# Optimization experiments

Measured on AMD Instinct MI355X. Metric: run time of the kernel, lower is better.

## Reference

```python
import jax, jax.numpy as jnp
import numpy as np

IMG_SIZE = 500
FM = 31
RATIOS = [1.0, 2.0, 0.5]
SCALES = [128, 256, 512]
PRE_NMS_TOPN = 6000
POST_NMS_TOPN = 1500
IOU_THRESHOLD = 0.7
VARIANCES = (0.1, 0.1, 0.2, 0.2)
BATCH = 64
TOTAL_ANCHORS = FM * FM * len(RATIOS) * len(SCALES)  # 8649


def generate_anchors():
    # normalized [y1, x1, y2, x2] anchors on a FM x FM grid
    stride = 1.0 / FM
    ctr = (np.arange(FM, dtype=np.float32) + 0.5) * stride
    cx, cy = np.meshgrid(ctr, ctr)
    centers = np.stack([cy.ravel(), cx.ravel()], axis=-1)  # [FM*FM, 2] (cy, cx)
    hs, ws = [], []
    for scale in SCALES:
        for ratio in RATIOS:
            ws.append((scale * np.sqrt(ratio)) / IMG_SIZE)
            hs.append((scale / np.sqrt(ratio)) / IMG_SIZE)
    hw = np.stack([np.array(hs, np.float32), np.array(ws, np.float32)], axis=-1)  # [9, 2]
    mins = centers[:, None, :] - hw[None] / 2.0
    maxs = centers[:, None, :] + hw[None] / 2.0
    boxes = np.concatenate([mins, maxs], axis=-1).reshape(-1, 4)  # [A, 4]
    return np.clip(boxes, 0.0, 1.0).astype(np.float32)


def delta_to_bbox(anchors, deltas):
    # anchors: [A,4], deltas: [B,A,4] (dy, dx, dh, dw) -> [B,A,4] (y1,x1,y2,x2)
    anc_h = anchors[:, 2] - anchors[:, 0]
    anc_w = anchors[:, 3] - anchors[:, 1]
    anc_cy = anchors[:, 0] + 0.5 * anc_h
    anc_cx = anchors[:, 1] + 0.5 * anc_w
    h = jnp.exp(deltas[..., 2]) * anc_h
    w = jnp.exp(deltas[..., 3]) * anc_w
    cy = deltas[..., 0] * anc_h + anc_cy
    cx = deltas[..., 1] * anc_w + anc_cx
    return jnp.stack([cy - 0.5 * h, cx - 0.5 * w, cy + 0.5 * h, cx + 0.5 * w], axis=-1)


def pairwise_iou_one_vs_all(sel_box, boxes):
    # sel_box: [B,1,4], boxes: [B,N,4] -> iou [B,N]
    y1 = jnp.maximum(sel_box[..., 0], boxes[..., 0])
    x1 = jnp.maximum(sel_box[..., 1], boxes[..., 1])
    y2 = jnp.minimum(sel_box[..., 2], boxes[..., 2])
    x2 = jnp.minimum(sel_box[..., 3], boxes[..., 3])
    inter = jnp.maximum(y2 - y1, 0.0) * jnp.maximum(x2 - x1, 0.0)
    area_s = (sel_box[..., 2] - sel_box[..., 0]) * (sel_box[..., 3] - sel_box[..., 1])
    area_b = (boxes[..., 2] - boxes[..., 0]) * (boxes[..., 3] - boxes[..., 1])
    return inter / (area_s + area_b - inter + 1e-9)


def batched_greedy_nms(boxes, scores, max_out, iou_threshold):
    # boxes [B,N,4], scores [B,N]; greedy NMS, vectorized over batch, scan over picks
    B, N, _ = boxes.shape

    def step(active, _):
        masked = jnp.where(active, scores, -jnp.inf)            # [B,N]
        idx = jnp.argmax(masked, axis=1)                         # [B]
        sel_score = jnp.take_along_axis(masked, idx[:, None], axis=1)[:, 0]
        sel_box = jnp.take_along_axis(boxes, idx[:, None, None], axis=1)  # [B,1,4]
        iou = pairwise_iou_one_vs_all(sel_box, boxes)            # [B,N]
        active = active & (iou <= iou_threshold)
        valid = jnp.isfinite(sel_score)
        out_box = jnp.where(valid[:, None], sel_box[:, 0, :], 0.0)
        out_score = jnp.where(valid, sel_score, 0.0)
        return active, (out_box, out_score)

    active0 = jnp.ones((B, N), dtype=bool)
    _, (out_boxes, out_scores) = jax.lax.scan(step, active0, None, length=max_out)
    out_boxes = jnp.transpose(out_boxes, (1, 0, 2))   # [B,max_out,4]
    out_scores = jnp.transpose(out_scores, (1, 0))    # [B,max_out]
    # tf.image.combined_non_max_suppression clips output boxes to [0,1] by default
    return jnp.clip(out_boxes, 0.0, 1.0), out_scores


def setup_inputs() -> dict:
    key = jax.random.key(0)
    k1, k2, k3 = jax.random.split(key, 3)
    rpn_bbox_deltas = jax.random.normal(k1, (BATCH, FM, FM, 36), dtype=jnp.float32)
    rpn_probs = jax.random.uniform(k2, (BATCH, FM, FM, 9), dtype=jnp.float32)
    gt_labels = jax.random.randint(k3, (BATCH, 10), 0, 20).astype(jnp.int64)
    anchors = jnp.asarray(generate_anchors())
    return {"rpn_bbox_deltas": rpn_bbox_deltas, "rpn_probs": rpn_probs,
            "gt_labels": gt_labels, "anchors": anchors}


def reference(rpn_bbox_deltas, rpn_probs, gt_labels, anchors):
    B = rpn_bbox_deltas.shape[0]
    A = anchors.shape[0]
    variances = jnp.asarray(VARIANCES, dtype=rpn_bbox_deltas.dtype)
    deltas = rpn_bbox_deltas.reshape(B, A, 4) * variances
    probs = rpn_probs.reshape(B, A)
    rpn_bboxes = delta_to_bbox(anchors, deltas)              # [B,A,4]
    top_scores, top_idx = jax.lax.top_k(probs, PRE_NMS_TOPN)  # sorted desc
    top_boxes = jnp.take_along_axis(rpn_bboxes, top_idx[:, :, None], axis=1)
    roi_bboxes, roi_scores = batched_greedy_nms(top_boxes, top_scores,
                                                POST_NMS_TOPN, IOU_THRESHOLD)
    return roi_bboxes, roi_scores
```

## Files before the change

kernel.cpp:

```cpp
#include <hip/hip_runtime.h>
#include <math.h>

typedef unsigned int u32;
typedef unsigned short u16;
typedef unsigned long long u64;

#define BATCH 64
#define A_TOT 8649
#define TOPN  6000
#define POST  1500
#define NB    4096
#define NT    512
#define NWAVE 8
#define NSLOT 12
#define NCHUNK 94
#define HOR   16u
#define ENTSTEP 64u
#define DONEBIT 0x80000000u
#define CNTMASK 0x7FFFFFFFu
#define GUARD_MAX (1 << 18)

#define LDS_BYTES 106496

__global__ __launch_bounds__(NT, 2) void roibbox_kernel(
    const float* __restrict__ deltas,
    const float* __restrict__ probs,
    const float* __restrict__ anchors,
    float* __restrict__ out)
{
    #pragma clang fp contract(off)
    __shared__ alignas(16) char smem[LDS_BYTES];
    u64*    keysL   = (u64*)   (smem + 0);
    u32*    bucketA = (u32*)   (smem + 69632);
    u32*    bucketB = (u32*)   (smem + 86016);
    u32*    stemp   = (u32*)   (smem + 102400);
    float4* ringL   = (float4*)(smem + 69632);
    u16*    ppL     = (u16*)   (smem + 93632);
    u32*    ctrlP   = (u32*)   (smem + 105632);
    u32*    ctrlF   = (u32*)   (smem + 105636);
    u32*    bmL     = (u32*)   (smem + 105640);

    const int tid = threadIdx.x;
    const int b   = blockIdx.x;
    const u32 lane = (u32)tid & 63u;
    const u32 w    = (u32)tid >> 6;
    const float* pb = probs + (size_t)b * A_TOT;

    #pragma unroll
    for (int i = 0; i < NB/NT; ++i) bucketA[tid + i*NT] = 0u;
    __syncthreads();

    for (int j = tid; j < A_TOT; j += NT) {
        float s = pb[j];
        int bkt = (int)(s * (float)NB);
        bkt = (NB-1) - min(max(bkt, 0), NB-1);
        atomicAdd(&bucketA[bkt], 1u);
    }
    __syncthreads();

    {
        int base8 = tid << 3;
        u32 c[8]; u32 ms = 0;
        #pragma unroll
        for (int i = 0; i < 8; ++i) { c[i] = bucketA[base8+i]; ms += c[i]; }
        stemp[tid] = ms;
        __syncthreads();
        int src = 0;
        for (int off = 1; off < NT; off <<= 1) {
            u32 v = stemp[src*NT + tid];
            if (tid >= off) v += stemp[src*NT + tid - off];
            stemp[(src^1)*NT + tid] = v;
            __syncthreads();
            src ^= 1;
        }
        u32 excl = stemp[src*NT + tid] - ms;
        #pragma unroll
        for (int i = 0; i < 8; ++i) {
            bucketA[base8+i] = excl; bucketB[base8+i] = excl; excl += c[i];
        }
    }
    __syncthreads();

    for (int j = tid; j < A_TOT; j += NT) {
        float s = pb[j];
        int bkt = (int)(s * (float)NB);
        bkt = (NB-1) - min(max(bkt, 0), NB-1);
        u32 pos = atomicAdd(&bucketB[bkt], 1u);
        keysL[pos] = ((u64)__float_as_uint(s) << 32) | (u64)(~(u32)j);
    }
    __syncthreads();

    for (int bkt = tid; bkt < NB; bkt += NT) {
        int begin = (int)bucketA[bkt], end = (int)bucketB[bkt];
        for (int k = begin + 1; k < end; ++k) {
            u64 key = keysL[k];
            int m = k - 1;
            while (m >= begin && keysL[m] < key) { keysL[m+1] = keysL[m]; --m; }
            keysL[m+1] = key;
        }
    }
    __syncthreads();

    float ry1[NSLOT], rx1[NSLOT], ry2[NSLOT], rx2[NSLOT], rA[NSLOT];
    u32 mask = 0;
    #pragma unroll
    for (int i = 0; i < NSLOT; ++i) {
        u32 s = (u32)i*8u + w;
        u32 r = s*64u + lane;
        ry1[i]=0.f; rx1[i]=0.f; ry2[i]=0.f; rx2[i]=0.f; rA[i]=0.f;
        if (s < NCHUNK && r < TOPN) {
            u64 k = keysL[r];
            u32 aidx = ~((u32)k);
            float4 av = *(const float4*)(anchors + (size_t)aidx * 4);
            float4 dv = *(const float4*)(deltas + ((size_t)b * A_TOT + aidx) * 4);
            float d0 = dv.x*0.1f, d1 = dv.y*0.1f, d2 = dv.z*0.2f, d3 = dv.w*0.2f;
            float ah = av.z - av.x, aw = av.w - av.y;
            float acy = av.x + 0.5f*ah, acx = av.y + 0.5f*aw;
            float h  = (float)exp((double)d2) * ah;
            float wd = (float)exp((double)d3) * aw;
            float cy = d0*ah + acy;
            float cx = d1*aw + acx;
            ry1[i] = cy - 0.5f*h;  rx1[i] = cx - 0.5f*wd;
            ry2[i] = cy + 0.5f*h;  rx2[i] = cx + 0.5f*wd;
            rA[i]  = (ry2[i]-ry1[i])*(rx2[i]-rx1[i]);
            mask |= 1u << i;
        }
    }

    for (int j = tid; j < TOPN/2; j += NT) ((u32*)ppL)[j] = 0xFFFFFFFFu;
    if (tid == 0) { *ctrlP = 0u; *ctrlF = 0u; bmL[0] = 0u; bmL[1] = 0u; bmL[2] = 0xC0000000u; }
    __syncthreads();

    const double MTHR = (double)0.7f + 0x1p-25;

    auto scanNext = [&](u32 from) -> u32 {
        for (u32 k = from >> 5; k < 3u; ++k) {
            u32 v = ~__hip_atomic_load(&bmL[k], __ATOMIC_RELAXED, __HIP_MEMORY_SCOPE_WORKGROUP);
            if (k == (from >> 5)) v &= ~((1u << (from & 31u)) - 1u);
            if (v) return k*32u + (u32)__builtin_ctz(v);
        }
        return 96u;
    };

    #define APPLY(i, e, sA)  do {                                              \
        float yy1 = fmaxf((e).x, ry1[i]);                                      \
        float xx1 = fmaxf((e).y, rx1[i]);                                      \
        float yy2 = fminf((e).z, ry2[i]);                                      \
        float xx2 = fminf((e).w, rx2[i]);                                      \
        float inter = fmaxf(yy2 - yy1, 0.f) * fmaxf(xx2 - xx1, 0.f);           \
        float den = (((sA) + rA[i]) - inter) + 1e-9f;     \
        if ((double)inter >= MTHR * (double)den) mask &= ~(1u << (i));         \
    } while (0)

    #define ENTRUN(I, tgt) do {                                                \
        u32 q_ = entC;                                                         \
        if (q_ < (tgt)) {                                                      \
            float4 e0_ = ringL[q_];                                            \
            float4 e1_ = (q_+1 < (tgt)) ? ringL[q_+1] : e0_;                   \
            for (; q_ < (tgt); ++q_) {                                         \
                float4 e_ = e0_; e0_ = e1_;                                    \
                if (q_+2 < (tgt)) e1_ = ringL[q_+2];                           \
                float sA_ = (e_.z - e_.x) * (e_.w - e_.y);                     \
                APPLY(I, e_, sA_);                                             \
            }                                                                  \
            entC = (tgt);                                                      \
        }                                                                      \
    } while (0)

    u32 hmask = 0;
    u32 consumed = 0;
    u32 hnext = 0;
    u32 entSlot = NSLOT;
    u32 entC = 0;

    auto ent_step = [&](u32 tgt) {
        switch (entSlot) {
            case 0:  ENTRUN(0,  tgt); break;
            case 1:  ENTRUN(1,  tgt); break;
            case 2:  ENTRUN(2,  tgt); break;
            case 3:  ENTRUN(3,  tgt); break;
            case 4:  ENTRUN(4,  tgt); break;
            case 5:  ENTRUN(5,  tgt); break;
            case 6:  ENTRUN(6,  tgt); break;
            case 7:  ENTRUN(7,  tgt); break;
            case 8:  ENTRUN(8,  tgt); break;
            case 9:  ENTRUN(9,  tgt); break;
            case 10: ENTRUN(10, tgt); break;
            default: ENTRUN(11, tgt); break;
        }
    };
    auto ent_promote = [&]() {
        u32 es = entSlot;
        if (__ballot((mask >> es) & 1u)) hmask |= 1u << es;
        else if (lane == 0) {
            u32 s = es*8u + w;
            __hip_atomic_fetch_or(&bmL[s >> 5], 1u << (s & 31u),
                                  __ATOMIC_RELAXED, __HIP_MEMORY_SCOPE_WORKGROUP);
        }
        entSlot = NSLOT;
    };
    auto group_consume = [&](u32 cnt) {
        if (consumed >= cnt) return;
        if (hmask) {
            u32 q = consumed;
            float4 e0 = ringL[q];
            float4 e1 = (q+1 < cnt) ? ringL[q+1] : e0;
            for (; q < cnt; ++q) {
                float4 e = e0; e0 = e1;
                if (q+2 < cnt) e1 = ringL[q+2];
                float sA = (e.z - e.x) * (e.w - e.y);
                #pragma unroll
                for (int i = 0; i < NSLOT; ++i)
                    if ((hmask >> i) & 1u) APPLY(i, e, sA);
            }
            u32 nh = hmask;
            #pragma unroll
            for (int i = 0; i < NSLOT; ++i)
                if ((hmask >> i) & 1u)
                    if (!__ballot((mask >> i) & 1u)) nh &= ~(1u << i);
            u32 diedm = hmask & ~nh;
            hmask = nh;
            if (diedm && lane == 0) {
                #pragma unroll
                for (int i = 0; i < NSLOT; ++i)
                    if ((diedm >> i) & 1u) {
                        u32 s = (u32)i*8u + w;
                        __hip_atomic_fetch_or(&bmL[s >> 5], 1u << (s & 31u),
                                              __ATOMIC_RELAXED, __HIP_MEMORY_SCOPE_WORKGROUP);
                    }
            }
        }
        consumed = cnt;
    };

    for (int g = 0; g < GUARD_MAX; ++g) {
        u32 pv = __hip_atomic_load(ctrlP, __ATOMIC_ACQUIRE, __HIP_MEMORY_SCOPE_WORKGROUP);
        if (pv & DONEBIT) break;
        u32 cnt = pv & CNTMASK;
        u32 f = __hip_atomic_load(ctrlF, __ATOMIC_ACQUIRE, __HIP_MEMORY_SCOPE_WORKGROUP);

        if ((f & 7u) == w && f < NCHUNK) {
            u32 pv2 = __hip_atomic_load(ctrlP, __ATOMIC_ACQUIRE, __HIP_MEMORY_SCOPE_WORKGROUP);
            if (pv2 & DONEBIT) break;
            u32 cnt2 = pv2 & CNTMASK;
            group_consume(cnt2);
            u32 fi = f >> 3;
            if (entSlot < NSLOT && entSlot <= fi) { ent_step(consumed); ent_promote(); }
            if (hnext <= fi) {
                u32 svS = entSlot, svC = entC;
                while (hnext <= fi) {
                    entSlot = hnext++; entC = 0;
                    ent_step(consumed); ent_promote();
                }
                entSlot = svS; entC = svC;
            }
            if ((hmask >> fi) & 1u) {
                float cy1, cx1, cy2, cx2, cA_;
                switch (fi) {
                    case 0:  cy1=ry1[0];  cx1=rx1[0];  cy2=ry2[0];  cx2=rx2[0];  cA_=rA[0];  break;
                    case 1:  cy1=ry1[1];  cx1=rx1[1];  cy2=ry2[1];  cx2=rx2[1];  cA_=rA[1];  break;
                    case 2:  cy1=ry1[2];  cx1=rx1[2];  cy2=ry2[2];  cx2=rx2[2];  cA_=rA[2];  break;
                    case 3:  cy1=ry1[3];  cx1=rx1[3];  cy2=ry2[3];  cx2=rx2[3];  cA_=rA[3];  break;
                    case 4:  cy1=ry1[4];  cx1=rx1[4];  cy2=ry2[4];  cx2=rx2[4];  cA_=rA[4];  break;
                    case 5:  cy1=ry1[5];  cx1=rx1[5];  cy2=ry2[5];  cx2=rx2[5];  cA_=rA[5];  break;
                    case 6:  cy1=ry1[6];  cx1=rx1[6];  cy2=ry2[6];  cx2=rx2[6];  cA_=rA[6];  break;
                    case 7:  cy1=ry1[7];  cx1=rx1[7];  cy2=ry2[7];  cx2=rx2[7];  cA_=rA[7];  break;
                    case 8:  cy1=ry1[8];  cx1=rx1[8];  cy2=ry2[8];  cx2=rx2[8];  cA_=rA[8];  break;
                    case 9:  cy1=ry1[9];  cx1=rx1[9];  cy2=ry2[9];  cx2=rx2[9];  cA_=rA[9];  break;
                    case 10: cy1=ry1[10]; cx1=rx1[10]; cy2=ry2[10]; cx2=rx2[10]; cA_=rA[10]; break;
                    default: cy1=ry1[11]; cx1=rx1[11]; cy2=ry2[11]; cx2=rx2[11]; cA_=rA[11]; break;
                }
                u64 am = __ballot((mask >> fi) & 1u);
                mask &= ~(1u << fi);
                hmask &= ~(1u << fi);
                u32 pc = cnt2;
                bool alldone = false;
                __builtin_amdgcn_s_setprio(1);
                while (true) {
                    if (!am) {
                        if (lane == 0)
                            __hip_atomic_fetch_or(&bmL[f >> 5], 1u << (f & 31u),
                                                  __ATOMIC_RELAXED, __HIP_MEMORY_SCOPE_WORKGROUP);
                        u32 nxt = scanNext(f + 1u);
                        if (nxt >= NCHUNK) {
                            if (lane == 0)
                                __hip_atomic_store(ctrlP, pc | DONEBIT, __ATOMIC_RELEASE,
                                                   __HIP_MEMORY_SCOPE_WORKGROUP);
                            alldone = true;
                        } else if (lane == 0) {
                            __hip_atomic_store(ctrlF, nxt, __ATOMIC_RELEASE,
                                               __HIP_MEMORY_SCOPE_WORKGROUP);
                        }
                        break;
                    }
                    u32 ol = (u32)__builtin_ctzll(am);
                    float sy1 = __uint_as_float((u32)__builtin_amdgcn_readlane((int)__float_as_uint(cy1), (int)ol));
                    float sx1 = __uint_as_float((u32)__builtin_amdgcn_readlane((int)__float_as_uint(cx1), (int)ol));
                    float sy2 = __uint_as_float((u32)__builtin_amdgcn_readlane((int)__float_as_uint(cy2), (int)ol));
                    float sx2 = __uint_as_float((u32)__builtin_amdgcn_readlane((int)__float_as_uint(cx2), (int)ol));
                    if (lane == ol) {
                        ppL[f*64u + ol] = (u16)pc;
                        ringL[pc] = make_float4(cy1, cx1, cy2, cx2);
                    }
                    float sA = (sy2 - sy1) * (sx2 - sx1);
                    float yy1 = fmaxf(sy1, cy1);
                    float xx1 = fmaxf(sx1, cx1);
                    float yy2 = fminf(sy2, cy2);
                    float xx2 = fminf(sx2, cx2);
                    float inter = fmaxf(yy2 - yy1, 0.f) * fmaxf(xx2 - xx1, 0.f);
                    float den = ((sA + cA_) - inter) + 1e-9f;
                    u64 supp = __ballot((double)inter >= MTHR * (double)den);
                    am &= ~supp;
                    ++pc;
                    u32 val = pc | ((pc >= POST) ? DONEBIT : 0u);
                    if (lane == 0)
                        __hip_atomic_store(ctrlP, val, __ATOMIC_RELEASE,
                                           __HIP_MEMORY_SCOPE_WORKGROUP);
                    if (pc >= POST) { alldone = true; break; }
                }
                __builtin_amdgcn_s_setprio(0);
                if (alldone) break;
                continue;
            } else {
                u32 nxt = scanNext(f + 1u);
                if (nxt >= NCHUNK) {
                    if (lane == 0)
                        __hip_atomic_store(ctrlP, cnt2 | DONEBIT, __ATOMIC_RELEASE,
                                           __HIP_MEMORY_SCOPE_WORKGROUP);
                    break;
                }
                if (lane == 0)
                    __hip_atomic_store(ctrlF, nxt, __ATOMIC_RELEASE,
                                       __HIP_MEMORY_SCOPE_WORKGROUP);
                continue;
            }
        }

        bool idle = true;
        if (cnt > consumed) { group_consume(cnt); idle = false; }
        if (entSlot < NSLOT) {
            if (entC < consumed) {
                u32 tgt = consumed; u32 lim = entC + ENTSTEP;
                if (lim < tgt) tgt = lim;
                ent_step(tgt);
                idle = false;
            }
            if (entC == consumed) ent_promote();
        } else if (hnext < NSLOT) {
            u32 s = (u32)hnext*8u + w;
            if (s >= NCHUNK) hnext = NSLOT;
            else if (s <= f + HOR) {
                entSlot = hnext++; entC = 0;
                if (entC == consumed) ent_promote();
                idle = false;
            }
        }
        if (idle) __builtin_amdgcn_s_sleep(2);
    }
    __syncthreads();
    u32 pend = (*ctrlP) & CNTMASK;

    const size_t sbase = (size_t)BATCH * POST * 4;
    #pragma unroll
    for (int i = 0; i < NSLOT; ++i) {
        u32 s = (u32)i*8u + w;
        u32 r = s*64u + lane;
        if (s < NCHUNK && r < TOPN) {
            u32 v = (u32)ppL[r];
            if (v != 0xFFFFu) {
                size_t row = (size_t)b * POST + v;
                float* ob = out + row * 4;
                ob[0] = fminf(fmaxf(ry1[i], 0.f), 1.f);
                ob[1] = fminf(fmaxf(rx1[i], 0.f), 1.f);
                ob[2] = fminf(fmaxf(ry2[i], 0.f), 1.f);
                ob[3] = fminf(fmaxf(rx2[i], 0.f), 1.f);
                out[sbase + row] = __uint_as_float((u32)(keysL[r] >> 32));
            }
        }
    }
    for (int p = (int)pend + tid; p < POST; p += NT) {
        size_t row = (size_t)b * POST + p;
        float* ob = out + row * 4;
        ob[0]=0.f; ob[1]=0.f; ob[2]=0.f; ob[3]=0.f;
        out[sbase + row] = 0.f;
    }
    #undef APPLY
    #undef ENTRUN
}

extern "C" void kernel_launch(void* const* d_in, const int* in_sizes, int n_in,
                              void* d_out, int out_size, void* d_ws, size_t ws_size,
                              hipStream_t stream) {
    const float* deltas  = (const float*)d_in[0];
    const float* probs   = (const float*)d_in[1];
    const float* anchors = (const float*)d_in[3];
    float* out = (float*)d_out;

    roibbox_kernel<<<dim3(BATCH), dim3(NT), 0, stream>>>(deltas, probs, anchors, out);
}
```

Baseline: 1.269 ms.

## Batch NMS progress publishing, fast-forward owner slot, and add exponential idle backoff

The owning wave now publishes the selected-count control word only every fourth selection and when its chunk is exhausted, instead of after every pick. It also applies pending ring entries to just its own active slot rather than consuming the whole group before processing. Idle waves back off with growing sleep intervals when nothing has changed since the last poll. Together these aim to cut LDS atomic traffic and polling contention on the serial NMS critical path, at the cost of other waves seeing progress later and possibly waking up late.

Result: no change. 1.271 ms (+0.2%).

```diff
diff --git a/kernel.cpp b/kernel.cpp
--- a/kernel.cpp
+++ b/kernel.cpp
@@ -167,6 +167,20 @@
         }                                                                      \
     } while (0)
 
+    #define FFRUN(I, from, to) do {                                            \
+        u32 q_ = (from);                                                       \
+        if (q_ < (to)) {                                                       \
+            float4 e0_ = ringL[q_];                                            \
+            float4 e1_ = (q_+1 < (to)) ? ringL[q_+1] : e0_;                    \
+            for (; q_ < (to); ++q_) {                                          \
+                float4 e_ = e0_; e0_ = e1_;                                    \
+                if (q_+2 < (to)) e1_ = ringL[q_+2];                            \
+                float sA_ = (e_.z - e_.x) * (e_.w - e_.y);                     \
+                APPLY(I, e_, sA_);                                             \
+            }                                                                  \
+        }                                                                      \
+    } while (0)
+
     u32 hmask = 0;
     u32 consumed = 0;
     u32 hnext = 0;
@@ -187,6 +201,22 @@
             case 9:  ENTRUN(9,  tgt); break;
             case 10: ENTRUN(10, tgt); break;
             default: ENTRUN(11, tgt); break;
+        }
+    };
+    auto ff_step = [&](u32 fi, u32 from, u32 to) {
+        switch (fi) {
+            case 0:  FFRUN(0,  from, to); break;
+            case 1:  FFRUN(1,  from, to); break;
+            case 2:  FFRUN(2,  from, to); break;
+            case 3:  FFRUN(3,  from, to); break;
+            case 4:  FFRUN(4,  from, to); break;
+            case 5:  FFRUN(5,  from, to); break;
+            case 6:  FFRUN(6,  from, to); break;
+            case 7:  FFRUN(7,  from, to); break;
+            case 8:  FFRUN(8,  from, to); break;
+            case 9:  FFRUN(9,  from, to); break;
+            case 10: FFRUN(10, from, to); break;
+            default: FFRUN(11, from, to); break;
         }
     };
     auto ent_promote = [&]() {
@@ -233,6 +263,7 @@
         consumed = cnt;
     };
 
+    u32 lastCnt = 0xFFFFFFFFu, lastF = 0xFFFFFFFFu, bk = 0;
     for (int g = 0; g < GUARD_MAX; ++g) {
         u32 pv = __hip_atomic_load(ctrlP, __ATOMIC_ACQUIRE, __HIP_MEMORY_SCOPE_WORKGROUP);
         if (pv & DONEBIT) break;
@@ -243,7 +274,6 @@
             u32 pv2 = __hip_atomic_load(ctrlP, __ATOMIC_ACQUIRE, __HIP_MEMORY_SCOPE_WORKGROUP);
             if (pv2 & DONEBIT) break;
             u32 cnt2 = pv2 & CNTMASK;
-            group_consume(cnt2);
             u32 fi = f >> 3;
             if (entSlot < NSLOT && entSlot <= fi) { ent_step(consumed); ent_promote(); }
             if (hnext <= fi) {
@@ -255,6 +285,7 @@
                 entSlot = svS; entC = svC;
             }
             if ((hmask >> fi) & 1u) {
+                ff_step(fi, consumed, cnt2);
                 float cy1, cx1, cy2, cx2, cA_;
                 switch (fi) {
                     case 0:  cy1=ry1[0];  cx1=rx1[0];  cy2=ry2[0];  cx2=rx2[0];  cA_=rA[0];  break;
@@ -278,9 +309,12 @@
                 __builtin_amdgcn_s_setprio(1);
                 while (true) {
                     if (!am) {
-                        if (lane == 0)
+                        if (lane == 0) {
+                            __hip_atomic_store(ctrlP, pc, __ATOMIC_RELEASE,
+                                               __HIP_MEMORY_SCOPE_WORKGROUP);
                             __hip_atomic_fetch_or(&bmL[f >> 5], 1u << (f & 31u),
                                                   __ATOMIC_RELAXED, __HIP_MEMORY_SCOPE_WORKGROUP);
+                        }
                         u32 nxt = scanNext(f + 1u);
                         if (nxt >= NCHUNK) {
                             if (lane == 0)
@@ -312,14 +346,19 @@
                     u64 supp = __ballot((double)inter >= MTHR * (double)den);
                     am &= ~supp;
                     ++pc;
-                    u32 val = pc | ((pc >= POST) ? DONEBIT : 0u);
-                    if (lane == 0)
-                        __hip_atomic_store(ctrlP, val, __ATOMIC_RELEASE,
+                    if (pc >= POST) {
+                        if (lane == 0)
+                            __hip_atomic_store(ctrlP, pc | DONEBIT, __ATOMIC_RELEASE,
+                                               __HIP_MEMORY_SCOPE_WORKGROUP);
+                        alldone = true; break;
+                    }
+                    if ((pc & 3u) == 0u && lane == 0)
+                        __hip_atomic_store(ctrlP, pc, __ATOMIC_RELEASE,
                                            __HIP_MEMORY_SCOPE_WORKGROUP);
-                    if (pc >= POST) { alldone = true; break; }
                 }
                 __builtin_amdgcn_s_setprio(0);
                 if (alldone) break;
+                lastCnt = 0xFFFFFFFFu; bk = 0;
                 continue;
             } else {
                 u32 nxt = scanNext(f + 1u);
@@ -332,18 +371,19 @@
                 if (lane == 0)
                     __hip_atomic_store(ctrlF, nxt, __ATOMIC_RELEASE,
                                        __HIP_MEMORY_SCOPE_WORKGROUP);
+                bk = 0;
                 continue;
             }
         }
 
-        bool idle = true;
-        if (cnt > consumed) { group_consume(cnt); idle = false; }
+        bool work = false;
+        if (cnt > consumed) { group_consume(cnt); work = true; }
         if (entSlot < NSLOT) {
             if (entC < consumed) {
                 u32 tgt = consumed; u32 lim = entC + ENTSTEP;
                 if (lim < tgt) tgt = lim;
                 ent_step(tgt);
-                idle = false;
+                work = true;
             }
             if (entC == consumed) ent_promote();
         } else if (hnext < NSLOT) {
@@ -352,10 +392,19 @@
             else if (s <= f + HOR) {
                 entSlot = hnext++; entC = 0;
                 if (entC == consumed) ent_promote();
-                idle = false;
-            }
-        }
-        if (idle) __builtin_amdgcn_s_sleep(2);
+                work = true;
+            }
+        }
+        if (!work && cnt == lastCnt && f == lastF) {
+            if      (bk == 0) __builtin_amdgcn_s_sleep(1);
+            else if (bk == 1) __builtin_amdgcn_s_sleep(2);
+            else if (bk == 2) __builtin_amdgcn_s_sleep(4);
+            else              __builtin_amdgcn_s_sleep(8);
+            if (bk < 3) ++bk;
+        } else {
+            bk = 0;
+        }
+        lastCnt = cnt; lastF = f;
     }
     __syncthreads();
     u32 pend = (*ctrlP) & CNTMASK;
@@ -386,6 +435,7 @@
     }
     #undef APPLY
     #undef ENTRUN
+    #undef FFRUN
 }
 
 extern "C" void kernel_launch(void* const* d_in, const int* in_sizes, int n_in,
```
